# Kernel tuning notes

Measured on AMD Instinct MI355X. Metric: run time of the kernel, lower is better.

Reference implementation:

```python
import jax, jax.numpy as jnp
import numpy as np
import math

B, H, W, CIN = 8, 64, 64, 192
INNER, K, N, P = 384, 2, 32, 64
NHK = INNER // P          # heads per scan direction = 6
NH = K * NHK              # total heads = 12
HID = 4 * CIN

def _silu(v):
    return v * jax.nn.sigmoid(v)

def setup_inputs() -> dict:
    key = jax.random.key(0)
    ks = jax.random.split(key, 12)
    x = jax.random.normal(ks[0], (B, H, W, CIN), jnp.float32)
    W_in = jax.random.normal(ks[1], (2 * INNER, CIN), jnp.float32) * 0.02
    conv_w = jax.random.normal(ks[2], (INNER, 1, 3, 3), jnp.float32) * 0.1
    conv_b = jnp.zeros((INNER,), jnp.float32)
    x_proj_weight = jax.random.normal(ks[3], (K, 2 * N + NHK, INNER), jnp.float32) * 0.02
    A_logs = jnp.log(jax.random.uniform(ks[4], (NH,), jnp.float32, 1.0, 16.0))
    Ds = jnp.ones((NH,), jnp.float32)
    u = jax.random.uniform(ks[5], (NH,), jnp.float32)
    dt = jnp.exp(u * (math.log(0.1) - math.log(0.001)) + math.log(0.001))
    dt = jnp.clip(dt, 1e-4, None)
    dt_bias = dt + jnp.log(-jnp.expm1(-dt))
    init_states = jnp.zeros((NH, P, N), jnp.float32)
    W_out = jax.random.normal(ks[6], (CIN, INNER), jnp.float32) * 0.02
    W1 = jax.random.normal(ks[7], (HID, CIN), jnp.float32) * 0.02
    b1 = jnp.zeros((HID,), jnp.float32)
    W2 = jax.random.normal(ks[8], (CIN, HID), jnp.float32) * 0.02
    b2 = jnp.zeros((CIN,), jnp.float32)
    return dict(x=x, W_in=W_in, conv_w=conv_w, conv_b=conv_b, x_proj_weight=x_proj_weight,
                A_logs=A_logs, Ds=Ds, dt_bias=dt_bias, init_states=init_states,
                W_out=W_out, W1=W1, b1=b1, W2=W2, b2=b2)

def reference(x, W_in, conv_w, conv_b, x_proj_weight, A_logs, Ds, dt_bias,
              init_states, W_out, W1, b1, W2, b2):
    Bb, Hh, Ww, Cin = x.shape
    L = Hh * Ww
    inner = W_in.shape[0] // 2
    shortcut = x
    # norm1 is identity (norm=None). in_proj (no bias), split into x and gate z
    xz = jnp.einsum('bhwc,dc->bhwd', x, W_in)
    xl, z = jnp.split(xz, 2, axis=-1)
    # depthwise conv (NCHW) + SiLU
    xc = jnp.transpose(xl, (0, 3, 1, 2))
    xc = jax.lax.conv_general_dilated(xc, conv_w, (1, 1), 'SAME',
                                      feature_group_count=inner,
                                      dimension_numbers=('NCHW', 'OIHW', 'NCHW'))
    xc = _silu(xc + conv_b[None, :, None, None])
    # cross scan: row-major and transposed (W-major) flattenings
    xs = jnp.stack([xc.reshape(Bb, inner, L),
                    jnp.transpose(xc, (0, 1, 3, 2)).reshape(Bb, inner, L)], axis=1)  # (B,K,inner,L)
    # project to B, C, dt per direction
    BCdt = jnp.einsum('bkdl,kcd->blkc', xs, x_proj_weight)  # (B,L,K,2N+NHK)
    Bs = BCdt[..., :N]                     # (B,L,K,N)
    Cs = BCdt[..., N:2 * N]                # (B,L,K,N)
    dt = BCdt[..., 2 * N:].reshape(Bb, L, NH)
    xh = jnp.transpose(xs, (0, 3, 1, 2)).reshape(Bb, L, NH, P)  # heads: k-major
    # Mamba2 selective scan (dt_softplus with bias)
    dt = jax.nn.softplus(dt + dt_bias)     # (B,L,NH)
    A = -jnp.exp(A_logs)                   # (NH,)
    da = jnp.exp(dt * A)                   # (B,L,NH)
    dtx = dt[..., None] * xh               # (B,L,NH,P)
    Bh = jnp.repeat(Bs, NHK, axis=2)       # (B,L,NH,N) group -> heads
    Ch = jnp.repeat(Cs, NHK, axis=2)
    h0 = jnp.broadcast_to(init_states, (Bb,) + init_states.shape)  # (B,NH,P,N)
    def step(h, inp):
        da_t, dtx_t, B_t, C_t = inp
        h = da_t[..., None, None] * h + dtx_t[..., None] * B_t[:, :, None, :]
        y_t = jnp.einsum('bhpn,bhn->bhp', h, C_t)
        return h, y_t
    _, ys = jax.lax.scan(step, h0, (jnp.moveaxis(da, 1, 0), jnp.moveaxis(dtx, 1, 0),
                                    jnp.moveaxis(Bh, 1, 0), jnp.moveaxis(Ch, 1, 0)))
    y = jnp.moveaxis(ys, 0, 1) + Ds[None, None, :, None] * xh  # (B,L,NH,P)
    out_y = jnp.transpose(y.reshape(Bb, L, K, inner), (0, 2, 3, 1))  # (B,K,inner,L)
    # scan_proj: undo each direction's flattening and sum
    y0 = out_y[:, 0].reshape(Bb, inner, Hh, Ww)
    y1 = jnp.transpose(out_y[:, 1].reshape(Bb, inner, Ww, Hh), (0, 1, 3, 2))
    yr = jnp.transpose((y0 + y1).reshape(Bb, inner, L), (0, 2, 1)).reshape(Bb, Hh, Ww, inner)
    # gate, out_proj, residual, MLP branch (dense is identity since in==out)
    yg = yr * _silu(z)
    out = shortcut + jnp.einsum('bhwd,cd->bhwc', yg, W_out)
    h1 = _silu(jnp.einsum('...c,dc->...d', out, W1) + b1)
    mlp = jnp.einsum('...d,cd->...c', h1, W2) + b2
    return out + mlp
```

## Files before the change

kernel.cpp:

```cpp
#include <hip/hip_runtime.h>
#include <math.h>

#define BB 8
#define HH 64
#define WW 64
#define CIN 192
#define INNER 384
#define LL 4096
#define NSTATE 32
#define PDIM 64
#define NHK 6
#define NHEADS 12
#define HID 768
#define CPROJ 70
#define QC 64
#define NC 64

#define WS_XLZ   0u
#define WS_XC    50331648u
#define WS_Y1    75497472u
#define WS_BCBF  100663296u
#define WS_DTRAW 109051904u
#define WS_DTV   119013376u
#define WS_CUMS  120586240u
#define WS_SHB   122159104u
#define WS_Y0    147324928u
#define WS_XBF   172490752u
#define WS_WINB  185073664u
#define WS_WPADB 185368576u
#define WS_WOUTB 185565184u
#define WS_W1B   185761792u
#define WS_W2B   186056704u
#define WS_REQ   186449920u

typedef __attribute__((ext_vector_type(8))) short short8;
typedef __attribute__((ext_vector_type(4))) float f32x4;

__device__ __forceinline__ float silu_f(float x) { return x / (1.f + __expf(-x)); }

__device__ __forceinline__ unsigned short f2bf(float f) {
    unsigned u = __float_as_uint(f);
    u += 0x7fffu + ((u >> 16) & 1u);
    return (unsigned short)(u >> 16);
}
__device__ __forceinline__ float bf2f(unsigned short u) {
    return __uint_as_float(((unsigned)u) << 16);
}

template<int AMODE>
__device__ __forceinline__ short8 load_a(const void* A, const unsigned short* Ay0,
                                         const unsigned short* Ay1, const unsigned short* Az,
                                         int row, int col, int Kd)
{
    if constexpr (AMODE == 0) {
        return *(const short8*)((const unsigned short*)A + (size_t)row * Kd + col);
    } else {
        const size_t yo = (size_t)row * INNER + col;
        const uint4 a  = *(const uint4*)(Ay0 + yo);
        const uint4 bv = *(const uint4*)(Ay1 + yo);
        const uint4 zv = *(const uint4*)(Az + (size_t)row * 768 + INNER + col);
        const unsigned ua[4]={a.x,a.y,a.z,a.w}, ub[4]={bv.x,bv.y,bv.z,bv.w}, uz[4]={zv.x,zv.y,zv.z,zv.w};
        short8 r;
        #pragma unroll
        for (int w2 = 0; w2 < 4; ++w2) {
            const float ylo = __uint_as_float(ua[w2] << 16) + __uint_as_float(ub[w2] << 16);
            const float yhi = __uint_as_float(ua[w2] & 0xffff0000u) + __uint_as_float(ub[w2] & 0xffff0000u);
            const float zlo = __uint_as_float(uz[w2] << 16);
            const float zhi = __uint_as_float(uz[w2] & 0xffff0000u);
            r[2*w2+0] = (short)f2bf(ylo * silu_f(zlo));
            r[2*w2+1] = (short)f2bf(yhi * silu_f(zhi));
        }
        return r;
    }
}

template<int EPI, int TRANSA, int AMODE>
__global__ __launch_bounds__(256)
void gemm_bf16(const void* __restrict__ A, const unsigned short* __restrict__ Wt,
               const float* __restrict__ bias, const float* __restrict__ res,
               float* __restrict__ Cf, unsigned short* __restrict__ Cb,
               const unsigned short* __restrict__ Ay0, const unsigned short* __restrict__ Ay1,
               const unsigned short* __restrict__ Az,
               int Kd, int ldc, int nmax)
{
    __shared__ __align__(16) short Als[128 * 64];
    __shared__ __align__(16) short Bls[128 * 64];
    const int tid = threadIdx.x;
    const int m0 = blockIdx.x * 128;
    const int n0 = blockIdx.y * 128;
    const int lane = tid & 63;
    const int wv = tid >> 6;
    const int wm = (wv >> 1) << 6;
    const int wn = (wv & 1) << 6;

    int am[4], ac[4];
    const unsigned short* gB[4];
    int lw[4];
    #pragma unroll
    for (int c = 0; c < 4; ++c) {
        const int idx = c * 256 + tid;
        const int row = idx >> 3;
        const int kb  = idx & 7;
        const int sb  = kb ^ (row & 7);
        lw[c] = row * 64 + sb * 8;
        int arow;
        const int mm = m0 + row;
        if (TRANSA) {
            const int bq = mm >> 12, lq = mm & 4095;
            arow = (bq << 12) + (((lq & 63) << 6) + (lq >> 6));
        } else {
            arow = mm;
        }
        am[c] = arow;
        ac[c] = kb * 8;
        gB[c] = Wt + (size_t)(n0 + row) * Kd + kb * 8;
    }

    f32x4 acc[4][4];
    #pragma unroll
    for (int i = 0; i < 4; ++i)
        #pragma unroll
        for (int j = 0; j < 4; ++j) acc[i][j] = (f32x4){0.f, 0.f, 0.f, 0.f};

    const int NT = Kd >> 6;
    short8 pA[4], pB[4];
    #pragma unroll
    for (int c = 0; c < 4; ++c) {
        pA[c] = load_a<AMODE>(A, Ay0, Ay1, Az, am[c], ac[c], Kd);
        pB[c] = *(const short8*)(gB[c]);
    }
    for (int kt = 0; kt < NT; ++kt) {
        __syncthreads();
        #pragma unroll
        for (int c = 0; c < 4; ++c) {
            *(short8*)&Als[lw[c]] = pA[c];
            *(short8*)&Bls[lw[c]] = pB[c];
        }
        __syncthreads();
        if (kt + 1 < NT) {
            #pragma unroll
            for (int c = 0; c < 4; ++c) {
                pA[c] = load_a<AMODE>(A, Ay0, Ay1, Az, am[c], ac[c] + (kt + 1) * 64, Kd);
                pB[c] = *(const short8*)(gB[c] + (kt + 1) * 64);
            }
        }
        #pragma unroll
        for (int ks = 0; ks < 2; ++ks) {
            short8 af[4], bfr[4];
            #pragma unroll
            for (int r = 0; r < 4; ++r) {
                const int rowa = wm + r * 16 + (lane & 15);
                const int rowb = wn + r * 16 + (lane & 15);
                const int kb = ks * 4 + (lane >> 4);
                af[r]  = *(const short8*)&Als[rowa * 64 + ((kb ^ (rowa & 7)) << 3)];
                bfr[r] = *(const short8*)&Bls[rowb * 64 + ((kb ^ (rowb & 7)) << 3)];
            }
            #pragma unroll
            for (int mr = 0; mr < 4; ++mr)
                #pragma unroll
                for (int nr = 0; nr < 4; ++nr)
                    acc[mr][nr] = __builtin_amdgcn_mfma_f32_16x16x32_bf16(af[mr], bfr[nr], acc[mr][nr], 0, 0, 0);
        }
    }
    #pragma unroll
    for (int mr = 0; mr < 4; ++mr) {
        #pragma unroll
        for (int nr = 0; nr < 4; ++nr) {
            const int n = n0 + wn + nr * 16 + (lane & 15);
            if (n >= nmax) continue;
            const int mb = m0 + wm + mr * 16 + ((lane >> 4) << 2);
            #pragma unroll
            for (int q = 0; q < 4; ++q) {
                const size_t off = (size_t)(mb + q) * ldc + n;
                float v = acc[mr][nr][q];
                if (EPI == 0) { Cf[off] = v; }
                else if (EPI == 1) { v = silu_f(v + bias[n]); Cb[off] = f2bf(v); }
                else if (EPI == 2) { v += bias[n] + res[off]; Cf[off] = v; }
                else if (EPI == 3) { v += res[off]; Cf[off] = v; Cb[off] = f2bf(v); }
                else if (EPI == 4) { Cb[off] = f2bf(v); }
            }
        }
    }
}

__global__ __launch_bounds__(256)
void gemm_bcdt(const unsigned short* __restrict__ A, const unsigned short* __restrict__ wpadb,
               float* __restrict__ dtraw, unsigned short* __restrict__ BCbf)
{
    __shared__ __align__(16) short Als[128 * 64];
    __shared__ __align__(16) short Bls[128 * 64];
    const int tid = threadIdx.x;
    const int m0 = blockIdx.x * 128;
    const int kk = blockIdx.y;
    const int lane = tid & 63;
    const int wv = tid >> 6;
    const int wm = (wv >> 1) << 6;
    const int wn = (wv & 1) << 6;
    const int Kd = INNER;
    const unsigned short* Wt = wpadb + (size_t)kk * 128 * INNER;

    int am[4], ac[4];
    const unsigned short* gB[4];
    int lw[4];
    #pragma unroll
    for (int c = 0; c < 4; ++c) {
        const int idx = c * 256 + tid;
        const int row = idx >> 3;
        const int kb  = idx & 7;
        const int sb  = kb ^ (row & 7);
        lw[c] = row * 64 + sb * 8;
        const int mm = m0 + row;
        int arow;
        if (kk) {
            const int bq = mm >> 12, lq = mm & 4095;
            arow = (bq << 12) + (((lq & 63) << 6) + (lq >> 6));
        } else {
            arow = mm;
        }
        am[c] = arow;
        ac[c] = kb * 8;
        gB[c] = Wt + (size_t)row * Kd + kb * 8;
    }

    f32x4 acc[4][4];
    #pragma unroll
    for (int i = 0; i < 4; ++i)
        #pragma unroll
        for (int j = 0; j < 4; ++j) acc[i][j] = (f32x4){0.f, 0.f, 0.f, 0.f};

    short8 pA[4], pB[4];
    #pragma unroll
    for (int c = 0; c < 4; ++c) {
        pA[c] = *(const short8*)(A + (size_t)am[c] * Kd + ac[c]);
        pB[c] = *(const short8*)(gB[c]);
    }
    for (int kt = 0; kt < 6; ++kt) {
        __syncthreads();
        #pragma unroll
        for (int c = 0; c < 4; ++c) {
            *(short8*)&Als[lw[c]] = pA[c];
            *(short8*)&Bls[lw[c]] = pB[c];
        }
        __syncthreads();
        if (kt + 1 < 6) {
            #pragma unroll
            for (int c = 0; c < 4; ++c) {
                pA[c] = *(const short8*)(A + (size_t)am[c] * Kd + ac[c] + (kt + 1) * 64);
                pB[c] = *(const short8*)(gB[c] + (kt + 1) * 64);
            }
        }
        #pragma unroll
        for (int ks = 0; ks < 2; ++ks) {
            short8 af[4], bfr[4];
            #pragma unroll
            for (int r = 0; r < 4; ++r) {
                const int rowa = wm + r * 16 + (lane & 15);
                const int rowb = wn + r * 16 + (lane & 15);
                const int kb = ks * 4 + (lane >> 4);
                af[r]  = *(const short8*)&Als[rowa * 64 + ((kb ^ (rowa & 7)) << 3)];
                bfr[r] = *(const short8*)&Bls[rowb * 64 + ((kb ^ (rowb & 7)) << 3)];
            }
            #pragma unroll
            for (int mr = 0; mr < 4; ++mr)
                #pragma unroll
                for (int nr = 0; nr < 4; ++nr)
                    acc[mr][nr] = __builtin_amdgcn_mfma_f32_16x16x32_bf16(af[mr], bfr[nr], acc[mr][nr], 0, 0, 0);
        }
    }
    float* Cf = dtraw + 6 * kk;
    unsigned short* Cb = BCbf + 64 * kk;
    #pragma unroll
    for (int mr = 0; mr < 4; ++mr) {
        #pragma unroll
        for (int nr = 0; nr < 4; ++nr) {
            const int n = wn + nr * 16 + (lane & 15);
            if (n >= CPROJ) continue;
            const int mb = m0 + wm + mr * 16 + ((lane >> 4) << 2);
            #pragma unroll
            for (int q = 0; q < 4; ++q) {
                const float v = acc[mr][nr][q];
                if (n < 64) Cb[(size_t)(mb + q) * 128 + n] = f2bf(v);
                else        Cf[(size_t)(mb + q) * 12 + (n - 64)] = v;
            }
        }
    }
}

__global__ __launch_bounds__(256)
void cvt_all_kernel(const float* __restrict__ x, const float* __restrict__ W_in,
                    const float* __restrict__ W1, const float* __restrict__ xpw,
                    const float* __restrict__ W_out, const float* __restrict__ W2,
                    unsigned short* __restrict__ x_bf,
                    unsigned short* __restrict__ Winb, unsigned short* __restrict__ W1b,
                    unsigned short* __restrict__ wpadb, unsigned short* __restrict__ Woutb,
                    unsigned short* __restrict__ W2b)
{
    int i = blockIdx.x * 256 + threadIdx.x;
    if (i < 6291456) { x_bf[i] = f2bf(x[i]); return; }
    i -= 6291456;
    if (i < 147456) { Winb[i] = f2bf(W_in[i]); return; }
    i -= 147456;
    if (i < 147456) { W1b[i] = f2bf(W1[i]); return; }
    i -= 147456;
    if (i < 98304) {
        const int d = i % 384;
        const int rr = (i / 384) & 127;
        const int k = i / 49152;
        wpadb[i] = (rr < CPROJ) ? f2bf(xpw[((size_t)k * CPROJ + rr) * 384 + d]) : (unsigned short)0;
        return;
    }
    i -= 98304;
    if (i < 98304) {
        const int rr = i / 384;
        Woutb[i] = (rr < CIN) ? f2bf(W_out[i]) : (unsigned short)0;
        return;
    }
    i -= 98304;
    if (i < 196608) {
        const int rr = i / 768;
        W2b[i] = (rr < CIN) ? f2bf(W2[i]) : (unsigned short)0;
    }
}

__global__ __launch_bounds__(256)
void conv_dw_kernel(const unsigned short* __restrict__ xlz, const float* __restrict__ cw,
                    const float* __restrict__ cb, unsigned short* __restrict__ xcbf)
{
    const int t = blockIdx.x * 256 + threadIdx.x;
    const int dv = t % 48;
    int r = t / 48;
    const int j  = r & 63;  r >>= 6;
    const int ib = r & 7;   r >>= 3;
    const int b  = r;
    const int d0 = dv * 8;
    const int i0 = ib * 8;

    float wreg[72];
    {
        const float4* w4 = (const float4*)(cw + d0 * 9);
        #pragma unroll
        for (int u = 0; u < 18; ++u) {
            const float4 v = w4[u];
            wreg[4*u+0]=v.x; wreg[4*u+1]=v.y; wreg[4*u+2]=v.z; wreg[4*u+3]=v.w;
        }
    }
    float bias[8];
    {
        const float4 b0 = *(const float4*)(cb + d0);
        const float4 b1 = *(const float4*)(cb + d0 + 4);
        bias[0]=b0.x; bias[1]=b0.y; bias[2]=b0.z; bias[3]=b0.w;
        bias[4]=b1.x; bias[5]=b1.y; bias[6]=b1.z; bias[7]=b1.w;
    }

    const unsigned short* base = xlz + ((size_t)b << 12) * 768 + d0;
    const int jok[3] = { (j - 1 >= 0), 1, (j + 1 < WW) };

    unsigned rm[3][4], r0[3][4], rp[3][4];
    #pragma unroll
    for (int cj = 0; cj < 3; ++cj) {
        uint4 vm = make_uint4(0,0,0,0), v0 = make_uint4(0,0,0,0);
        if (jok[cj]) {
            if (i0 - 1 >= 0) vm = *(const uint4*)(base + (size_t)((i0-1) * 64 + j - 1 + cj) * 768);
            v0 = *(const uint4*)(base + (size_t)(i0 * 64 + j - 1 + cj) * 768);
        }
        rm[cj][0]=vm.x; rm[cj][1]=vm.y; rm[cj][2]=vm.z; rm[cj][3]=vm.w;
        r0[cj][0]=v0.x; r0[cj][1]=v0.y; r0[cj][2]=v0.z; r0[cj][3]=v0.w;
    }

    #pragma unroll
    for (int ii = 0; ii < 8; ++ii) {
        const int i = i0 + ii;
        #pragma unroll
        for (int cj = 0; cj < 3; ++cj) {
            uint4 vp = make_uint4(0,0,0,0);
            if (jok[cj] && (i + 1 < HH))
                vp = *(const uint4*)(base + (size_t)((i+1) * 64 + j - 1 + cj) * 768);
            rp[cj][0]=vp.x; rp[cj][1]=vp.y; rp[cj][2]=vp.z; rp[cj][3]=vp.w;
        }
        float acc[8];
        #pragma unroll
        for (int ch = 0; ch < 8; ++ch) acc[ch] = bias[ch];
        #pragma unroll
        for (int cj = 0; cj < 3; ++cj) {
            #pragma unroll
            for (int w2 = 0; w2 < 4; ++w2) {
                acc[2*w2+0] = fmaf(__uint_as_float(rm[cj][w2] << 16),        wreg[(2*w2+0)*9 + cj],     acc[2*w2+0]);
                acc[2*w2+1] = fmaf(__uint_as_float(rm[cj][w2] & 0xffff0000u), wreg[(2*w2+1)*9 + cj],     acc[2*w2+1]);
                acc[2*w2+0] = fmaf(__uint_as_float(r0[cj][w2] << 16),        wreg[(2*w2+0)*9 + 3 + cj], acc[2*w2+0]);
                acc[2*w2+1] = fmaf(__uint_as_float(r0[cj][w2] & 0xffff0000u), wreg[(2*w2+1)*9 + 3 + cj], acc[2*w2+1]);
                acc[2*w2+0] = fmaf(__uint_as_float(rp[cj][w2] << 16),        wreg[(2*w2+0)*9 + 6 + cj], acc[2*w2+0]);
                acc[2*w2+1] = fmaf(__uint_as_float(rp[cj][w2] & 0xffff0000u), wreg[(2*w2+1)*9 + 6 + cj], acc[2*w2+1]);
            }
        }
        unsigned o[4];
        #pragma unroll
        for (int w2 = 0; w2 < 4; ++w2) {
            const unsigned lo = f2bf(silu_f(acc[2*w2+0]));
            const unsigned hi = f2bf(silu_f(acc[2*w2+1]));
            o[w2] = lo | (hi << 16);
        }
        *(uint4*)(xcbf + ((size_t)(b << 12) + (size_t)(i * 64 + j)) * INNER + d0) =
            make_uint4(o[0], o[1], o[2], o[3]);
        #pragma unroll
        for (int cj = 0; cj < 3; ++cj)
            #pragma unroll
            for (int w2 = 0; w2 < 4; ++w2) {
                rm[cj][w2] = r0[cj][w2];
                r0[cj][w2] = rp[cj][w2];
            }
    }
}

__global__ __launch_bounds__(256)
void dtcums_kernel(const float* __restrict__ dtraw, const float* __restrict__ dt_bias,
                   const float* __restrict__ A_logs,
                   float* __restrict__ dtv, float* __restrict__ cums)
{
    const int w = blockIdx.x * 4 + (threadIdx.x >> 6);
    const int lane = threadIdx.x & 63;
    const int b = w / (NHEADS * NC);
    const int rem = w - b * (NHEADS * NC);
    const int h = rem / NC;
    const int c = rem - h * NC;
    const int k = h / NHK;
    const int hq = h - k * NHK;
    const int l = c * QC + lane;
    const float dtr = dtraw[(((size_t)b * LL + l) * 2 + k) * 6 + hq];
    const float xx = dtr + dt_bias[h];
    const float sp = (xx > 20.f) ? xx : log1pf(expf(xx));
    float s = -expf(A_logs[h]) * sp;
    #pragma unroll
    for (int d = 1; d < 64; d <<= 1) {
        const float o = __shfl_up(s, d);
        if (lane >= d) s += o;
    }
    dtv[((size_t)b * LL + l) * NHEADS + h] = sp;
    cums[((size_t)b * LL + l) * NHEADS + h] = s;
}

__global__ __launch_bounds__(256)
void chunk_state_kernel(const unsigned short* __restrict__ xcbf, const unsigned short* __restrict__ BCbf,
                        const float* __restrict__ dtv, const float* __restrict__ cums,
                        unsigned short* __restrict__ SHb)
{
    __shared__ __align__(16) unsigned short Xb[PDIM][72];
    __shared__ __align__(16) unsigned short Bsc[NSTATE][72];
    __shared__ float cuS[QC], rs[QC];
    const int c = blockIdx.x, h = blockIdx.y, b = blockIdx.z;
    const int k = h / NHK;
    const int dch0 = (h - k * NHK) * PDIM;
    const int tid = threadIdx.x;
    const int lane = tid & 63;
    const int w = tid >> 6;

    #pragma unroll
    for (int r2 = 0; r2 < 2; ++r2) {
        const int idx = tid + r2 * 256;
        const int m = idx >> 3, pg = idx & 7;
        const int pos = (k == 0) ? (c * QC + m) : (m * QC + c);
        const uint4 v = *(const uint4*)(xcbf + (((size_t)b << 12) + pos) * INNER + dch0 + pg * 8);
        const unsigned ua[4] = {v.x, v.y, v.z, v.w};
        #pragma unroll
        for (int e2 = 0; e2 < 4; ++e2) {
            Xb[pg * 8 + 2*e2 + 0][m] = (unsigned short)(ua[e2] & 0xffffu);
            Xb[pg * 8 + 2*e2 + 1][m] = (unsigned short)(ua[e2] >> 16);
        }
    }
    if (tid < QC)
        cuS[tid] = cums[((size_t)b * LL + c * QC + tid) * NHEADS + h];
    __syncthreads();
    if (tid < QC)
        rs[tid] = dtv[((size_t)b * LL + c * QC + tid) * NHEADS + h] * __expf(cuS[QC-1] - cuS[tid]);
    __syncthreads();
    #pragma unroll
    for (int r = 0; r < 8; ++r) {
        const int idx = tid + r * 256;
        const int m = idx >> 5, n = idx & 31;
        Bsc[n][m] = f2bf(rs[m] * bf2f(BCbf[(((size_t)b * LL + c * QC + m) * 2 + k) * 64 + n]));
    }
    __syncthreads();

    const int rowf = lane & 15;
    const int ko   = lane >> 4;
    f32x4 acc[2] = {{0.f,0.f,0.f,0.f},{0.f,0.f,0.f,0.f}};
    #pragma unroll
    for (int ks = 0; ks < 2; ++ks) {
        const short8 af = *(const short8*)&Xb[w * 16 + rowf][ks * 32 + ko * 8];
        #pragma unroll
        for (int nt = 0; nt < 2; ++nt) {
            const short8 bfr = *(const short8*)&Bsc[nt * 16 + rowf][ks * 32 + ko * 8];
            acc[nt] = __builtin_amdgcn_mfma_f32_16x16x32_bf16(af, bfr, acc[nt], 0, 0, 0);
        }
    }
    unsigned short* base = SHb + ((((size_t)b * NHEADS + h) * NC + c) * PDIM) * NSTATE;
    #pragma unroll
    for (int nt = 0; nt < 2; ++nt) {
        #pragma unroll
        for (int q = 0; q < 4; ++q) {
            const int p = w * 16 + ko * 4 + q;
            base[p * NSTATE + nt * 16 + rowf] = f2bf(acc[nt][q]);
        }
    }
}

__global__ __launch_bounds__(64)
void state_scan_kernel(unsigned short* __restrict__ SHb, const float* __restrict__ cums,
                       const float* __restrict__ init_states)
{
    __shared__ float decays[NC];
    const int g = blockIdx.x;
    const int bh = g >> 2;
    const int quarter = g & 3;
    const int b = bh / NHEADS;
    const int h = bh % NHEADS;
    const int tid = threadIdx.x;
    decays[tid] = __expf(cums[((size_t)b * LL + tid * QC + QC - 1) * NHEADS + h]);
    __syncthreads();
    const int p = quarter * 16 + (tid >> 2);
    const int nb = (tid & 3) * 8;
    float hs[8];
    {
        const float* is = init_states + ((size_t)h * PDIM + p) * NSTATE + nb;
        #pragma unroll
        for (int i = 0; i < 8; ++i) hs[i] = is[i];
    }
    unsigned short* base = SHb + (((size_t)b * NHEADS + h) * NC) * (PDIM * NSTATE) + p * NSTATE + nb;
    for (int c = 0; c < NC; ++c) {
        unsigned short* slot = base + (size_t)c * (PDIM * NSTATE);
        const uint4 sv = *(const uint4*)slot;
        const unsigned ua[4] = {sv.x, sv.y, sv.z, sv.w};
        unsigned o[4];
        #pragma unroll
        for (int w2 = 0; w2 < 4; ++w2)
            o[w2] = (unsigned)f2bf(hs[2*w2]) | ((unsigned)f2bf(hs[2*w2+1]) << 16);
        *(uint4*)slot = make_uint4(o[0], o[1], o[2], o[3]);
        const float dc = decays[c];
        #pragma unroll
        for (int w2 = 0; w2 < 4; ++w2) {
            hs[2*w2+0] = fmaf(dc, hs[2*w2+0], __uint_as_float(ua[w2] << 16));
            hs[2*w2+1] = fmaf(dc, hs[2*w2+1], __uint_as_float(ua[w2] & 0xffff0000u));
        }
    }
}

__global__ __launch_bounds__(256)
void intra_kernel(const unsigned short* __restrict__ xcbf, const unsigned short* __restrict__ BCbf,
                  const float* __restrict__ dtv, const float* __restrict__ cums,
                  const unsigned short* __restrict__ SHb, const float* __restrict__ Ds,
                  unsigned short* __restrict__ y0, unsigned short* __restrict__ y1)
{
    __shared__ __align__(16) unsigned short Bs[QC][40];
    __shared__ __align__(16) unsigned short Cs[QC][40];
    __shared__ __align__(16) unsigned short Hs[PDIM][40];
    __shared__ __align__(16) unsigned short Xb[PDIM][72];
    __shared__ __align__(16) unsigned short Gb[QC][72];
    __shared__ float cuS[QC], dtS[QC], Ei[QC];
    const int c = blockIdx.x, h = blockIdx.y, b = blockIdx.z;
    const int k = h / NHK;
    const int dch0 = (h - k * NHK) * PDIM;
    const int tid = threadIdx.x;
    const int lane = tid & 63;
    const int w = tid >> 6;

    #pragma unroll
    for (int r2 = 0; r2 < 2; ++r2) {
        const int idx = tid + r2 * 256;
        const int m = idx >> 3, pg = idx & 7;
        const int pos = (k == 0) ? (c * QC + m) : (m * QC + c);
        const uint4 v = *(const uint4*)(xcbf + (((size_t)b << 12) + pos) * INNER + dch0 + pg * 8);
        const unsigned ua[4] = {v.x, v.y, v.z, v.w};
        #pragma unroll
        for (int e2 = 0; e2 < 4; ++e2) {
            Xb[pg * 8 + 2*e2 + 0][m] = (unsigned short)(ua[e2] & 0xffffu);
            Xb[pg * 8 + 2*e2 + 1][m] = (unsigned short)(ua[e2] >> 16);
        }
    }
    #pragma unroll
    for (int r = 0; r < 2; ++r) {
        const int idx = tid + r * 256;
        const int i = idx >> 3, ch = idx & 7;
        const uint4 v = *(const uint4*)(BCbf + (((size_t)b * LL + c * QC + i) * 2 + k) * 64 + ch * 8);
        if (ch < 4) *(uint4*)&Bs[i][ch * 8] = v;
        else        *(uint4*)&Cs[i][(ch - 4) * 8] = v;
    }
    {
        const int p = tid >> 2, ch = tid & 3;
        *(uint4*)&Hs[p][ch * 8] =
            *(const uint4*)(SHb + ((((size_t)b * NHEADS + h) * NC + c) * PDIM + p) * NSTATE + ch * 8);
    }
    if (tid < QC) {
        const size_t o = ((size_t)b * LL + c * QC + tid) * NHEADS + h;
        const float cu = cums[o];
        cuS[tid] = cu;
        dtS[tid] = dtv[o];
        Ei[tid]  = __expf(cu);
    }
    __syncthreads();

    const int rowf = lane & 15;
    const int ko   = lane >> 4;
    const short8 cfrag = *(const short8*)&Cs[w * 16 + rowf][ko * 8];

    f32x4 graw[4];
    #pragma unroll
    for (int mt = 0; mt < 4; ++mt) {
        const short8 bfrag = *(const short8*)&Bs[mt * 16 + rowf][ko * 8];
        graw[mt] = __builtin_amdgcn_mfma_f32_16x16x32_bf16(cfrag, bfrag, (f32x4){0.f,0.f,0.f,0.f}, 0, 0, 0);
    }
    #pragma unroll
    for (int mt = 0; mt < 4; ++mt) {
        const int m = mt * 16 + rowf;
        const float cum = cuS[m];
        const float dtm = dtS[m];
        #pragma unroll
        for (int q = 0; q < 4; ++q) {
            const int i = w * 16 + ko * 4 + q;
            float g = 0.f;
            if (m <= i) g = __expf(fminf(cuS[i] - cum, 0.f)) * dtm * graw[mt][q];
            Gb[i][m] = f2bf(g);
        }
    }
    f32x4 acc[4];
    #pragma unroll
    for (int pt = 0; pt < 4; ++pt) {
        const short8 hfrag = *(const short8*)&Hs[pt * 16 + rowf][ko * 8];
        acc[pt] = __builtin_amdgcn_mfma_f32_16x16x32_bf16(cfrag, hfrag, (f32x4){0.f,0.f,0.f,0.f}, 0, 0, 0);
    }
    const float Dh = Ds[h];
    #pragma unroll
    for (int pt = 0; pt < 4; ++pt) {
        const int p = pt * 16 + rowf;
        #pragma unroll
        for (int q = 0; q < 4; ++q) {
            const int i = w * 16 + ko * 4 + q;
            acc[pt][q] = acc[pt][q] * Ei[i] + Dh * bf2f(Xb[p][i]);
        }
    }
    #pragma unroll
    for (int ks = 0; ks < 2; ++ks) {
        const short8 gfrag = *(const short8*)&Gb[w * 16 + rowf][ks * 32 + ko * 8];
        #pragma unroll
        for (int pt = 0; pt < 4; ++pt) {
            const short8 xfrag = *(const short8*)&Xb[pt * 16 + rowf][ks * 32 + ko * 8];
            acc[pt] = __builtin_amdgcn_mfma_f32_16x16x32_bf16(gfrag, xfrag, acc[pt], 0, 0, 0);
        }
    }
    unsigned short* yk = (k == 0) ? y0 : y1;
    #pragma unroll
    for (int pt = 0; pt < 4; ++pt) {
        const int p = pt * 16 + rowf;
        #pragma unroll
        for (int q = 0; q < 4; ++q) {
            const int i = w * 16 + ko * 4 + q;
            const int pos = (k == 0) ? (c * QC + i) : (i * QC + c);
            yk[(((size_t)b << 12) + pos) * INNER + dch0 + p] = f2bf(acc[pt][q]);
        }
    }
}

__global__ __launch_bounds__(256)
void report_ws_kernel(float* __restrict__ out, int n, float val)
{
    const int e = blockIdx.x * 256 + threadIdx.x;
    if (e < n) out[e] = val;
}

extern "C" void kernel_launch(void* const* d_in, const int* in_sizes, int n_in,
                              void* d_out, int out_size, void* d_ws, size_t ws_size,
                              hipStream_t stream)
{
    const float* x          = (const float*)d_in[0];
    const float* W_in       = (const float*)d_in[1];
    const float* conv_w     = (const float*)d_in[2];
    const float* conv_b     = (const float*)d_in[3];
    const float* xpw        = (const float*)d_in[4];
    const float* A_logs     = (const float*)d_in[5];
    const float* Ds         = (const float*)d_in[6];
    const float* dt_bias    = (const float*)d_in[7];
    const float* init_states= (const float*)d_in[8];
    const float* W_out      = (const float*)d_in[9];
    const float* W1         = (const float*)d_in[10];
    const float* b1         = (const float*)d_in[11];
    const float* W2         = (const float*)d_in[12];
    const float* b2         = (const float*)d_in[13];
    float* out = (float*)d_out;

    if (ws_size < (size_t)WS_REQ) {
        const float mib = (float)((double)ws_size / 1048576.0);
        report_ws_kernel<<<(out_size + 255) / 256, 256, 0, stream>>>(out, out_size, mib);
        return;
    }

    char* ws = (char*)d_ws;
    unsigned short* xlz   = (unsigned short*)(ws + WS_XLZ);
    unsigned short* xc_bf = (unsigned short*)(ws + WS_XC);
    unsigned short* y1    = (unsigned short*)(ws + WS_Y1);
    unsigned short* BCbf  = (unsigned short*)(ws + WS_BCBF);
    float* dtraw = (float*)(ws + WS_DTRAW);
    float* dtv   = (float*)(ws + WS_DTV);
    float* cums  = (float*)(ws + WS_CUMS);
    unsigned short* SHb   = (unsigned short*)(ws + WS_SHB);
    unsigned short* y0    = (unsigned short*)(ws + WS_Y0);
    unsigned short* x_bf  = (unsigned short*)(ws + WS_XBF);
    unsigned short* Winb  = (unsigned short*)(ws + WS_WINB);
    unsigned short* wpadb = (unsigned short*)(ws + WS_WPADB);
    unsigned short* Woutb = (unsigned short*)(ws + WS_WOUTB);
    unsigned short* W1b   = (unsigned short*)(ws + WS_W1B);
    unsigned short* W2b   = (unsigned short*)(ws + WS_W2B);
    unsigned short* out_bf = (unsigned short*)(ws + WS_BCBF);
    unsigned short* h1_bf  = (unsigned short*)(ws + WS_XLZ);

    const int M = BB * LL;

    cvt_all_kernel<<<(6979584 + 255) / 256, 256, 0, stream>>>(x, W_in, W1, xpw, W_out, W2,
                                                              x_bf, Winb, W1b, wpadb, Woutb, W2b);

    gemm_bf16<4,0,0><<<dim3(M/128, HID/128), 256, 0, stream>>>(x_bf, Winb, nullptr, nullptr, nullptr, xlz,
                                                               nullptr, nullptr, nullptr, CIN, HID, HID);

    conv_dw_kernel<<<196608 / 256, 256, 0, stream>>>(xlz, conv_w, conv_b, xc_bf);

    gemm_bcdt<<<dim3(M/128, 2), 256, 0, stream>>>(xc_bf, wpadb, dtraw, BCbf);

    dtcums_kernel<<<(BB * NHEADS * NC) / 4, 256, 0, stream>>>(dtraw, dt_bias, A_logs, dtv, cums);

    chunk_state_kernel<<<dim3(NC, NHEADS, BB), 256, 0, stream>>>(xc_bf, BCbf, dtv, cums, SHb);
    state_scan_kernel<<<BB * NHEADS * 4, 64, 0, stream>>>(SHb, cums, init_states);
    intra_kernel<<<dim3(NC, NHEADS, BB), 256, 0, stream>>>(xc_bf, BCbf, dtv, cums, SHb, Ds, y0, y1);

    gemm_bf16<3,0,2><<<dim3(M/128, 2), 256, 0, stream>>>(nullptr, Woutb, nullptr, x, out, out_bf,
                                                         y0, y1, xlz, INNER, CIN, CIN);

    gemm_bf16<1,0,0><<<dim3(M/128, HID/128), 256, 0, stream>>>(out_bf, W1b, b1, nullptr, nullptr, h1_bf,
                                                               nullptr, nullptr, nullptr, CIN, HID, HID);

    gemm_bf16<2,0,0><<<dim3(M/128, 2), 256, 0, stream>>>(h1_bf, W2b, b2, out, out, nullptr,
                                                         nullptr, nullptr, nullptr, HID, CIN, CIN);
}
```

Baseline: 233.1 us.

## Swizzle LDS tiles in chunk_state/intra and split state scan finer with prefetch

The transposed bf16 tiles (Xb, Bsc) in chunk_state_kernel and intra_kernel are now written and read through an XOR swizzle on 8-element column groups, to reduce LDS bank conflicts on the transposing stores and the MFMA fragment reads. state_scan_kernel now runs twice as many blocks, each thread owning 4 state elements instead of 8, and prefetches the next chunk's value before the dependent FMA chain so the serial 64-step loop waits less on memory latency. The change adds index arithmetic, and the narrower per-thread loads are less wide.

```diff
diff --git a/kernel.cpp b/kernel.cpp
--- a/kernel.cpp
+++ b/kernel.cpp
@@ -460,10 +460,11 @@
         const int pos = (k == 0) ? (c * QC + m) : (m * QC + c);
         const uint4 v = *(const uint4*)(xcbf + (((size_t)b << 12) + pos) * INNER + dch0 + pg * 8);
         const unsigned ua[4] = {v.x, v.y, v.z, v.w};
+        const int mcol = (((m >> 3) ^ pg) << 3) + (m & 7);
         #pragma unroll
         for (int e2 = 0; e2 < 4; ++e2) {
-            Xb[pg * 8 + 2*e2 + 0][m] = (unsigned short)(ua[e2] & 0xffffu);
-            Xb[pg * 8 + 2*e2 + 1][m] = (unsigned short)(ua[e2] >> 16);
+            Xb[pg * 8 + 2*e2 + 0][mcol] = (unsigned short)(ua[e2] & 0xffffu);
+            Xb[pg * 8 + 2*e2 + 1][mcol] = (unsigned short)(ua[e2] >> 16);
         }
     }
     if (tid < QC)
@@ -476,19 +477,22 @@
     for (int r = 0; r < 8; ++r) {
         const int idx = tid + r * 256;
         const int m = idx >> 5, n = idx & 31;
-        Bsc[n][m] = f2bf(rs[m] * bf2f(BCbf[(((size_t)b * LL + c * QC + m) * 2 + k) * 64 + n]));
+        Bsc[n][(((m >> 3) ^ (n >> 3)) << 3) + (m & 7)] =
+            f2bf(rs[m] * bf2f(BCbf[(((size_t)b * LL + c * QC + m) * 2 + k) * 64 + n]));
     }
     __syncthreads();
 
     const int rowf = lane & 15;
     const int ko   = lane >> 4;
+    const int xsw = (w * 2 + (rowf >> 3)) & 7;
     f32x4 acc[2] = {{0.f,0.f,0.f,0.f},{0.f,0.f,0.f,0.f}};
     #pragma unroll
     for (int ks = 0; ks < 2; ++ks) {
-        const short8 af = *(const short8*)&Xb[w * 16 + rowf][ks * 32 + ko * 8];
+        const short8 af = *(const short8*)&Xb[w * 16 + rowf][((ks * 4 + ko) ^ xsw) << 3];
         #pragma unroll
         for (int nt = 0; nt < 2; ++nt) {
-            const short8 bfr = *(const short8*)&Bsc[nt * 16 + rowf][ks * 32 + ko * 8];
+            const int bsw = (nt * 2 + (rowf >> 3)) & 7;
+            const short8 bfr = *(const short8*)&Bsc[nt * 16 + rowf][((ks * 4 + ko) ^ bsw) << 3];
             acc[nt] = __builtin_amdgcn_mfma_f32_16x16x32_bf16(af, bfr, acc[nt], 0, 0, 0);
         }
     }
@@ -509,37 +513,35 @@
 {
     __shared__ float decays[NC];
     const int g = blockIdx.x;
-    const int bh = g >> 2;
-    const int quarter = g & 3;
+    const int bh = g >> 3;
+    const int oct = g & 7;
     const int b = bh / NHEADS;
     const int h = bh % NHEADS;
     const int tid = threadIdx.x;
     decays[tid] = __expf(cums[((size_t)b * LL + tid * QC + QC - 1) * NHEADS + h]);
     __syncthreads();
-    const int p = quarter * 16 + (tid >> 2);
-    const int nb = (tid & 3) * 8;
-    float hs[8];
+    const int p  = oct * 8 + (tid >> 3);
+    const int nb = (tid & 7) * 4;
+    float hs[4];
     {
         const float* is = init_states + ((size_t)h * PDIM + p) * NSTATE + nb;
-        #pragma unroll
-        for (int i = 0; i < 8; ++i) hs[i] = is[i];
+        hs[0]=is[0]; hs[1]=is[1]; hs[2]=is[2]; hs[3]=is[3];
     }
     unsigned short* base = SHb + (((size_t)b * NHEADS + h) * NC) * (PDIM * NSTATE) + p * NSTATE + nb;
+    uint2 sv = *(const uint2*)base;
     for (int c = 0; c < NC; ++c) {
         unsigned short* slot = base + (size_t)c * (PDIM * NSTATE);
-        const uint4 sv = *(const uint4*)slot;
-        const unsigned ua[4] = {sv.x, sv.y, sv.z, sv.w};
-        unsigned o[4];
-        #pragma unroll
-        for (int w2 = 0; w2 < 4; ++w2)
-            o[w2] = (unsigned)f2bf(hs[2*w2]) | ((unsigned)f2bf(hs[2*w2+1]) << 16);
-        *(uint4*)slot = make_uint4(o[0], o[1], o[2], o[3]);
+        uint2 nx = make_uint2(0u, 0u);
+        if (c + 1 < NC) nx = *(const uint2*)(slot + PDIM * NSTATE);
+        const unsigned o0 = (unsigned)f2bf(hs[0]) | ((unsigned)f2bf(hs[1]) << 16);
+        const unsigned o1 = (unsigned)f2bf(hs[2]) | ((unsigned)f2bf(hs[3]) << 16);
+        *(uint2*)slot = make_uint2(o0, o1);
         const float dc = decays[c];
-        #pragma unroll
-        for (int w2 = 0; w2 < 4; ++w2) {
-            hs[2*w2+0] = fmaf(dc, hs[2*w2+0], __uint_as_float(ua[w2] << 16));
-            hs[2*w2+1] = fmaf(dc, hs[2*w2+1], __uint_as_float(ua[w2] & 0xffff0000u));
-        }
+        hs[0] = fmaf(dc, hs[0], __uint_as_float(sv.x << 16));
+        hs[1] = fmaf(dc, hs[1], __uint_as_float(sv.x & 0xffff0000u));
+        hs[2] = fmaf(dc, hs[2], __uint_as_float(sv.y << 16));
+        hs[3] = fmaf(dc, hs[3], __uint_as_float(sv.y & 0xffff0000u));
+        sv = nx;
     }
 }
 
@@ -569,10 +571,11 @@
         const int pos = (k == 0) ? (c * QC + m) : (m * QC + c);
         const uint4 v = *(const uint4*)(xcbf + (((size_t)b << 12) + pos) * INNER + dch0 + pg * 8);
         const unsigned ua[4] = {v.x, v.y, v.z, v.w};
+        const int mcol = (((m >> 3) ^ pg) << 3) + (m & 7);
         #pragma unroll
         for (int e2 = 0; e2 < 4; ++e2) {
-            Xb[pg * 8 + 2*e2 + 0][m] = (unsigned short)(ua[e2] & 0xffffu);
-            Xb[pg * 8 + 2*e2 + 1][m] = (unsigned short)(ua[e2] >> 16);
+            Xb[pg * 8 + 2*e2 + 0][mcol] = (unsigned short)(ua[e2] & 0xffffu);
+            Xb[pg * 8 + 2*e2 + 1][mcol] = (unsigned short)(ua[e2] >> 16);
         }
     }
     #pragma unroll
@@ -630,10 +633,11 @@
     #pragma unroll
     for (int pt = 0; pt < 4; ++pt) {
         const int p = pt * 16 + rowf;
+        const int xsw = (pt * 2 + (rowf >> 3)) & 7;
         #pragma unroll
         for (int q = 0; q < 4; ++q) {
             const int i = w * 16 + ko * 4 + q;
-            acc[pt][q] = acc[pt][q] * Ei[i] + Dh * bf2f(Xb[p][i]);
+            acc[pt][q] = acc[pt][q] * Ei[i] + Dh * bf2f(Xb[p][(((i >> 3) ^ xsw) << 3) + (i & 7)]);
         }
     }
     #pragma unroll
@@ -641,7 +645,8 @@
         const short8 gfrag = *(const short8*)&Gb[w * 16 + rowf][ks * 32 + ko * 8];
         #pragma unroll
         for (int pt = 0; pt < 4; ++pt) {
-            const short8 xfrag = *(const short8*)&Xb[pt * 16 + rowf][ks * 32 + ko * 8];
+            const int xsw = (pt * 2 + (rowf >> 3)) & 7;
+            const short8 xfrag = *(const short8*)&Xb[pt * 16 + rowf][((ks * 4 + ko) ^ xsw) << 3];
             acc[pt] = __builtin_amdgcn_mfma_f32_16x16x32_bf16(gfrag, xfrag, acc[pt], 0, 0, 0);
         }
     }
@@ -725,7 +730,7 @@
     dtcums_kernel<<<(BB * NHEADS * NC) / 4, 256, 0, stream>>>(dtraw, dt_bias, A_logs, dtv, cums);
 
     chunk_state_kernel<<<dim3(NC, NHEADS, BB), 256, 0, stream>>>(xc_bf, BCbf, dtv, cums, SHb);
-    state_scan_kernel<<<BB * NHEADS * 4, 64, 0, stream>>>(SHb, cums, init_states);
+    state_scan_kernel<<<BB * NHEADS * 8, 64, 0, stream>>>(SHb, cums, init_states);
     intra_kernel<<<dim3(NC, NHEADS, BB), 256, 0, stream>>>(xc_bf, BCbf, dtv, cums, SHb, Ds, y0, y1);
 
     gemm_bf16<3,0,2><<<dim3(M/128, 2), 256, 0, stream>>>(nullptr, Woutb, nullptr, x, out, out_bf,
```

New measurement: 220.8 us, median of 2. 5.3% less time.
